# Optimization experiments

Hardware: AMD Instinct MI355X
Metric: run time of the kernel (lower is better)

## Reference

```python
import jax, jax.numpy as jnp
import numpy as np

B, S = 128, 512
VOCAB, E, H, T = 100000, 100, 128, 10  # tagset_size=10 -> CRF over T-1=9 tags
HD = H // 2  # per-direction LSTM hidden


def setup_inputs():
    key = jax.random.key(0)
    ks = jax.random.split(key, 14)
    s = 0.08
    inputs = jax.random.randint(ks[0], (B, S), 1, VOCAB)
    tags = jax.random.randint(ks[1], (B, S), 1, T)  # valid after tags-1 shift
    mask = jnp.ones((B, S), dtype=bool)
    emb = (jax.random.normal(ks[2], (VOCAB, E)) * s).at[0].set(0.0)  # padding_idx=0 row zeroed
    Wih_f = jax.random.normal(ks[3], (4 * HD, E)) * s
    Whh_f = jax.random.normal(ks[4], (4 * HD, HD)) * s
    b_f = jax.random.normal(ks[5], (4 * HD,)) * s
    Wih_b = jax.random.normal(ks[6], (4 * HD, E)) * s
    Whh_b = jax.random.normal(ks[7], (4 * HD, HD)) * s
    b_b = jax.random.normal(ks[8], (4 * HD,)) * s
    W_out = jax.random.normal(ks[9], (T, H)) * s
    b_out = jax.random.normal(ks[10], (T,)) * s
    start = jax.random.normal(ks[11], (T - 1,)) * s
    end = jax.random.normal(ks[12], (T - 1,)) * s
    trans = jax.random.normal(ks[13], (T - 1, T - 1)) * s
    return dict(inputs=inputs, tags=tags, mask=mask, emb=emb,
                Wih_f=Wih_f, Whh_f=Whh_f, b_f=b_f,
                Wih_b=Wih_b, Whh_b=Whh_b, b_b=b_b,
                W_out=W_out, b_out=b_out, start=start, end=end, trans=trans)


def _lstm_dir(x, Wih, Whh, b, reverse):
    # x: [S, B, E] time-major; PyTorch gate order i,f,g,o; b = b_ih + b_hh
    h0 = jnp.zeros((x.shape[1], Whh.shape[1]), x.dtype)

    def step(carry, xt):
        h, c = carry
        gates = xt @ Wih.T + h @ Whh.T + b
        i, f, g, o = jnp.split(gates, 4, axis=-1)
        c = jax.nn.sigmoid(f) * c + jax.nn.sigmoid(i) * jnp.tanh(g)
        h = jax.nn.sigmoid(o) * jnp.tanh(c)
        return (h, c), h

    _, hs = jax.lax.scan(step, (h0, h0), x, reverse=reverse)
    return hs  # [S, B, HD]


def _crf_nll(em, tags, mask, start, end, trans):
    # Linear-chain CRF (torchcrf-style). em: [S,B,K], tags/mask: [S,B]
    pick = lambda e, t: jnp.take_along_axis(e, t[:, None], axis=-1)[:, 0]
    # numerator: score of the gold path
    score0 = start[tags[0]] + pick(em[0], tags[0])

    def num_step(sc, inp):
        em_t, t, tp, m = inp
        return sc + jnp.where(m, trans[tp, t] + pick(em_t, t), 0.0), None

    score, _ = jax.lax.scan(num_step, score0, (em[1:], tags[1:], tags[:-1], mask[1:]))
    last_idx = mask.sum(0).astype(jnp.int32) - 1
    last_tags = jnp.take_along_axis(tags, last_idx[None, :], axis=0)[0]
    score = score + end[last_tags]
    # denominator: forward algorithm (log partition)
    alpha0 = start[None, :] + em[0]  # [B,K]

    def fwd_step(alpha, inp):
        em_t, m = inp
        nxt = jax.nn.logsumexp(alpha[:, :, None] + trans[None, :, :] + em_t[:, None, :], axis=1)
        return jnp.where(m[:, None], nxt, alpha), None

    alpha, _ = jax.lax.scan(fwd_step, alpha0, (em[1:], mask[1:]))
    logZ = jax.nn.logsumexp(alpha + end[None, :], axis=1)
    return -(score - logZ).mean()  # loss = -log_likelihood.mean()


def _forward(inputs, tags, mask, emb, Wih_f, Whh_f, b_f, Wih_b, Whh_b, b_b, W_out, b_out, start, end, trans):
    x = emb[inputs].transpose(1, 0, 2)  # [S,B,E]
    h = jnp.concatenate([_lstm_dir(x, Wih_f, Whh_f, b_f, False),
                         _lstm_dir(x, Wih_b, Whh_b, b_b, True)], axis=-1)  # [S,B,H]
    # dropout is identity at eval; slice off tag 0 as in the module
    em = (h @ W_out.T + b_out)[:, :, 1:]  # [S,B,T-1]
    return _crf_nll(em, (tags - 1).T, mask.T, start, end, trans)


def reference(inputs, tags, mask, emb, Wih_f, Whh_f, b_f, Wih_b, Whh_b, b_b, W_out, b_out, start, end, trans):
    return _forward(inputs, tags, mask, emb, Wih_f, Whh_f, b_f, Wih_b, Whh_b, b_b, W_out, b_out, start, end, trans)
```

## Files before the change

kernel.cpp:

```cpp
#include <hip/hip_runtime.h>
#include <math.h>

#define SB 512
#define NB 128
#define HD 64

typedef _Float16 h2 __attribute__((ext_vector_type(2)));
union U4 { uint4 u; h2 h[4]; _Float16 f[8]; };
union U2 { uint2 u; _Float16 f[4]; };
union UH { unsigned u; _Float16 f[2]; };

__device__ __forceinline__ float frcp(float x) { return __builtin_amdgcn_rcpf(x); }
__device__ __forceinline__ float fsig(float x) { return frcp(1.0f + __expf(-x)); }
__device__ __forceinline__ float ftanh(float x) {
    float t = __expf(-2.0f * fabsf(x));
    float r = (1.0f - t) * frcp(1.0f + t);
    return copysignf(r, x);
}
__device__ __forceinline__ float fdot2(h2 a, h2 b, float c) {
    return __builtin_amdgcn_fdot2(a, b, c, false);
}

__global__ void prep_kernel(const float* __restrict__ Wih_f, const float* __restrict__ Wih_bb,
                            const float* __restrict__ Whh_f, const float* __restrict__ Whh_bb,
                            const float* __restrict__ b_f, const float* __restrict__ b_bb,
                            const float* __restrict__ trans,
                            unsigned* __restrict__ W2h, unsigned* __restrict__ whh_h,
                            float* __restrict__ bias2, float* __restrict__ Eexp)
{
    int idx = blockIdx.x * 256 + threadIdx.x;
    if (idx < 26624) {
        int col = idx / 52, d = idx - col * 52;
        int dir = col >> 8, r = col & 255, j = r >> 2, g = r & 3;
        const float* src = (dir ? Wih_bb : Wih_f) + (g * 64 + j) * 100;
        UH u; u.u = 0;
        if (d < 50) { u.f[0] = (_Float16)src[2 * d]; u.f[1] = (_Float16)src[2 * d + 1]; }
        W2h[idx] = u.u;
    } else if (idx < 43008) {
        int i2 = idx - 26624;
        int q = i2 & 3, j = (i2 >> 2) & 63, k4 = (i2 >> 8) & 7, g = (i2 >> 11) & 3, dir = i2 >> 13;
        int p = k4 * 4 + q;
        const float* src = (dir ? Whh_bb : Whh_f) + (g * 64 + j) * 64 + 2 * p;
        UH u; u.f[0] = (_Float16)src[0]; u.f[1] = (_Float16)src[1];
        whh_h[(((dir * 4 + g) * 8 + k4) * 64 + j) * 4 + q] = u.u;
    } else if (idx < 43520) {
        int col = idx - 43008;
        int dir = col >> 8, r = col & 255, j = r >> 2, g = r & 3;
        bias2[col] = (dir ? b_bb : b_f)[g * 64 + j];
    } else if (idx < 43601) {
        int i = idx - 43520;
        Eexp[i] = __expf(trans[i]);
    }
}

__global__ __launch_bounds__(256, 1) void gemm_kernel(
    const int* __restrict__ inputs, const float* __restrict__ emb,
    const unsigned* __restrict__ W2h, const float* __restrict__ bias2,
    _Float16* __restrict__ xgh)
{
    __shared__ __align__(16) unsigned sE[128 * 52];
    __shared__ __align__(16) unsigned sW[128 * 52];
    __shared__ int stok[128];
    const int bx = blockIdx.x;
    const int tt = bx >> 2;
    const int cb = (bx & 3) * 128;
    const int tid = threadIdx.x;

    if (tid < 128) stok[tid] = inputs[tid * SB + tt];
    for (int idx = tid; idx < 1664; idx += 256)
        ((uint4*)sW)[idx] = ((const uint4*)W2h)[cb * 13 + idx];
    __syncthreads();
    for (int idx = tid; idx < 6656; idx += 256) {
        int row = idx / 52, d = idx - row * 52;
        int token = stok[row];
        UH u; u.u = 0;
        if (d < 50) {
            const float* ep = emb + (size_t)token * 100 + 2 * d;
            u.f[0] = (_Float16)ep[0]; u.f[1] = (_Float16)ep[1];
        }
        sE[idx] = u.u;
    }
    __syncthreads();

    const int tx = tid & 15, ty = tid >> 4;
    float acc[8][8];
    #pragma unroll
    for (int r = 0; r < 8; ++r)
        #pragma unroll
        for (int i = 0; i < 8; ++i) acc[r][i] = 0.f;

    for (int kk = 0; kk < 13; ++kk) {
        U4 e[8], wv[8];
        #pragma unroll
        for (int r = 0; r < 8; ++r) e[r].u = ((const uint4*)sE)[(ty + 16 * r) * 13 + kk];
        #pragma unroll
        for (int i = 0; i < 8; ++i) wv[i].u = ((const uint4*)sW)[(tx + 16 * i) * 13 + kk];
        #pragma unroll
        for (int r = 0; r < 8; ++r)
            #pragma unroll
            for (int i = 0; i < 8; ++i) {
                float a = acc[r][i];
                #pragma unroll
                for (int q = 0; q < 4; ++q) a = fdot2(e[r].h[q], wv[i].h[q], a);
                acc[r][i] = a;
            }
    }

    #pragma unroll
    for (int i = 0; i < 8; ++i) {
        int col = cb + tx + 16 * i;
        float bc = bias2[col];
        #pragma unroll
        for (int r = 0; r < 8; ++r) {
            int row = tt * NB + ty + 16 * r;
            xgh[(size_t)row * 512 + col] = (_Float16)(acc[r][i] + bc);
        }
    }
}

__global__ __launch_bounds__(64, 1) void lstm_kernel(
    const _Float16* __restrict__ xgh, const unsigned* __restrict__ whh_h,
    float* __restrict__ h_all)
{
    const int blk = blockIdx.x;
    const int b = blk & (NB - 1);
    const int dir = blk >> 7;
    const int j = threadIdx.x;

    U4 w[4][8];
    const uint4* W4 = (const uint4*)whh_h;
    #pragma unroll
    for (int g = 0; g < 4; ++g)
        #pragma unroll
        for (int k4 = 0; k4 < 8; ++k4)
            w[g][k4].u = W4[((dir * 4 + g) * 8 + k4) * 64 + j];

    __shared__ __align__(16) _Float16 hbuf[64];
    hbuf[j] = (_Float16)0.f;
    float c = 0.f;

    const int t0 = dir ? (SB - 1) : 0;
    const ptrdiff_t xstride = (dir ? -1 : 1) * (ptrdiff_t)(NB * 512);
    const ptrdiff_t hstride = (dir ? -1 : 1) * (ptrdiff_t)(NB * 128);
    const _Float16* xp = xgh + ((size_t)(t0 * NB + b)) * 512 + dir * 256 + j * 4;
    float* hp = h_all + ((size_t)(t0 * NB + b)) * 128 + dir * HD + j;

    U2 p0, p1;
    p0.u = *(const uint2*)xp;
    p1.u = *(const uint2*)(xp + xstride);
    const _Float16* xq = xp + 2 * xstride;
    __syncthreads();

    for (int s = 0; s < SB; ++s) {
        float a0 = (float)p0.f[0], a1 = (float)p0.f[1];
        float a2 = (float)p0.f[2], a3 = (float)p0.f[3];
        p0 = p1;
        p1.u = *(const uint2*)xq;
        xq += xstride;

        U4 hv[8];
        #pragma unroll
        for (int k4 = 0; k4 < 8; ++k4) hv[k4].u = ((const uint4*)hbuf)[k4];
        #pragma unroll
        for (int k4 = 0; k4 < 8; ++k4)
            #pragma unroll
            for (int q = 0; q < 4; ++q) {
                a0 = fdot2(hv[k4].h[q], w[0][k4].h[q], a0);
                a1 = fdot2(hv[k4].h[q], w[1][k4].h[q], a1);
                a2 = fdot2(hv[k4].h[q], w[2][k4].h[q], a2);
                a3 = fdot2(hv[k4].h[q], w[3][k4].h[q], a3);
            }

        float ig = fsig(a0), fg = fsig(a1), gg = ftanh(a2), og = fsig(a3);
        c = fg * c + ig * gg;
        float h = og * ftanh(c);
        *hp = h;
        hp += hstride;
        hbuf[j] = (_Float16)h;
        __syncthreads();
    }
}

__global__ __launch_bounds__(128) void proj_kernel(
    const float* __restrict__ h_all, const float* __restrict__ W_out,
    const float* __restrict__ b_out, float* __restrict__ em3)
{
    __shared__ __align__(16) float sWo[9 * 128];
    __shared__ float sb[9];
    const int t = blockIdx.x, b = threadIdx.x;
    for (int idx = b; idx < 1152; idx += 128) sWo[idx] = W_out[128 + idx];
    if (b < 9) sb[b] = b_out[1 + b];
    __syncthreads();

    const float4* h4 = (const float4*)(h_all + ((size_t)t * NB + b) * 128);
    float acc[9];
    #pragma unroll
    for (int k = 0; k < 9; ++k) acc[k] = 0.f;
    for (int q = 0; q < 32; ++q) {
        float4 hv = h4[q];
        #pragma unroll
        for (int k = 0; k < 9; ++k) {
            float4 wv = ((const float4*)sWo)[k * 32 + q];
            acc[k] += hv.x * wv.x + hv.y * wv.y + hv.z * wv.z + hv.w * wv.w;
        }
    }
    float* dst = em3 + (size_t)b * (SB * 12) + t * 12;
    #pragma unroll
    for (int k = 0; k < 9; ++k) dst[k] = acc[k] + sb[k];
}

__global__ __launch_bounds__(64, 1) void crf_gold(
    const float* __restrict__ em3, const int* __restrict__ tags,
    const float* __restrict__ startv, const float* __restrict__ endv,
    const float* __restrict__ trans, float* __restrict__ gold)
{
    const int b = blockIdx.x, l = threadIdx.x;
    const int* tb = tags + (size_t)b * SB;
    const float* eb = em3 + (size_t)b * (SB * 12);
    float sc = 0.f;
    for (int t = l; t < SB; t += 64) {
        int tg = tb[t] - 1;
        if (t > 0) {
            int tp = tb[t - 1] - 1;
            sc += trans[tp * 9 + tg] + eb[t * 12 + tg];
        }
    }
    if (l == 0) {
        int tg0 = tb[0] - 1, tgl = tb[SB - 1] - 1;
        sc += startv[tg0] + eb[tg0] + endv[tgl];
    }
    #pragma unroll
    for (int off = 32; off > 0; off >>= 1) sc += __shfl_down(sc, off);
    if (l == 0) gold[b] = sc;
}

__global__ __launch_bounds__(256, 1) void crf_scan(
    const float* __restrict__ em3, const float* __restrict__ Eexp,
    float* __restrict__ Pws)
{
    const int lane = blockIdx.x * 256 + threadIdx.x;
    const int c = lane & 31, b = lane >> 5;

    float E[81];
    #pragma unroll
    for (int i = 0; i < 81; ++i) E[i] = Eexp[i];

    float P[81];
    #pragma unroll
    for (int i = 0; i < 81; ++i) P[i] = 0.f;
    #pragma unroll
    for (int i = 0; i < 9; ++i) P[i * 9 + i] = 1.f;
    float M = 0.f;

    const int t0 = 1 + 16 * c;
    const int nst = (t0 + 16 <= SB) ? 16 : (SB - t0);
    const float* ep = em3 + (size_t)b * (SB * 12) + t0 * 12;

    for (int s = 0; s < nst; ++s, ep += 12) {
        float4 e0 = *(const float4*)ep;
        float4 e1 = *(const float4*)(ep + 4);
        float e8 = ep[8];
        float ex[9] = { __expf(e0.x), __expf(e0.y), __expf(e0.z), __expf(e0.w),
                        __expf(e1.x), __expf(e1.y), __expf(e1.z), __expf(e1.w),
                        __expf(e8) };
        #pragma unroll
        for (int i = 0; i < 9; ++i) {
            float tmp[9];
            #pragma unroll
            for (int jj = 0; jj < 9; ++jj) tmp[jj] = P[i * 9] * E[jj];
            #pragma unroll
            for (int k = 1; k < 9; ++k)
                #pragma unroll
                for (int jj = 0; jj < 9; ++jj) tmp[jj] += P[i * 9 + k] * E[k * 9 + jj];
            #pragma unroll
            for (int jj = 0; jj < 9; ++jj) P[i * 9 + jj] = tmp[jj] * ex[jj];
        }
        if ((s & 3) == 3) {
            float mx = P[0];
            #pragma unroll
            for (int i = 1; i < 81; ++i) mx = fmaxf(mx, P[i]);
            M += __logf(mx);
            float r = frcp(mx);
            #pragma unroll
            for (int i = 0; i < 81; ++i) P[i] *= r;
        }
    }

    float* dst = Pws + (size_t)lane * 84;
    #pragma unroll
    for (int i = 0; i < 81; ++i) dst[i] = P[i];
    dst[81] = M;
}

__global__ __launch_bounds__(128, 1) void crf_combine(
    const float* __restrict__ em3, const float* __restrict__ Pws,
    const float* __restrict__ gold, const float* __restrict__ startv,
    const float* __restrict__ endv, float* __restrict__ out)
{
    const int b = threadIdx.x;
    float A[9], M = 0.f;
    {
        const float* eb = em3 + (size_t)b * (SB * 12);
        float4 e0 = *(const float4*)eb;
        float4 e1 = *(const float4*)(eb + 4);
        float e[9] = { e0.x, e0.y, e0.z, e0.w, e1.x, e1.y, e1.z, e1.w, eb[8] };
        #pragma unroll
        for (int k = 0; k < 9; ++k) A[k] = __expf(startv[k] + e[k]);
    }

    for (int c = 0; c < 32; ++c) {
        const float4* src = (const float4*)(Pws + ((size_t)b * 32 + c) * 84);
        float buf[84];
        #pragma unroll
        for (int q = 0; q < 21; ++q) {
            float4 v = src[q];
            buf[4 * q] = v.x; buf[4 * q + 1] = v.y; buf[4 * q + 2] = v.z; buf[4 * q + 3] = v.w;
        }
        float tmp[9];
        #pragma unroll
        for (int jj = 0; jj < 9; ++jj) tmp[jj] = A[0] * buf[jj];
        #pragma unroll
        for (int i = 1; i < 9; ++i)
            #pragma unroll
            for (int jj = 0; jj < 9; ++jj) tmp[jj] += A[i] * buf[i * 9 + jj];
        float mx = tmp[0];
        #pragma unroll
        for (int jj = 1; jj < 9; ++jj) mx = fmaxf(mx, tmp[jj]);
        M += __logf(mx) + buf[81];
        float r = frcp(mx);
        #pragma unroll
        for (int jj = 0; jj < 9; ++jj) A[jj] = tmp[jj] * r;
    }

    float Z = 0.f;
    #pragma unroll
    for (int k = 0; k < 9; ++k) Z += A[k] * __expf(endv[k]);
    float part = M + __logf(Z) - gold[b];

    #pragma unroll
    for (int off = 32; off > 0; off >>= 1) part += __shfl_down(part, off);
    __shared__ float sm[2];
    if ((b & 63) == 0) sm[b >> 6] = part;
    __syncthreads();
    if (b == 0) out[0] = (sm[0] + sm[1]) * (1.0f / NB);
}

extern "C" void kernel_launch(void* const* d_in, const int* in_sizes, int n_in,
                              void* d_out, int out_size, void* d_ws, size_t ws_size,
                              hipStream_t stream)
{
    const int*   inputs = (const int*)d_in[0];
    const int*   tags   = (const int*)d_in[1];
    const float* emb    = (const float*)d_in[3];
    const float* Wih_f  = (const float*)d_in[4];
    const float* Whh_f  = (const float*)d_in[5];
    const float* b_f    = (const float*)d_in[6];
    const float* Wih_b  = (const float*)d_in[7];
    const float* Whh_b  = (const float*)d_in[8];
    const float* b_b    = (const float*)d_in[9];
    const float* W_out  = (const float*)d_in[10];
    const float* b_out  = (const float*)d_in[11];
    const float* startv = (const float*)d_in[12];
    const float* endv   = (const float*)d_in[13];
    const float* transv = (const float*)d_in[14];

    char* w = (char*)d_ws;
    float* h_all   = (float*)w;     w += (size_t)SB * NB * 128 * 4;
    _Float16* xgh  = (_Float16*)w;  w += (size_t)SB * NB * 512 * 2;
    float* em3     = (float*)w;     w += (size_t)NB * SB * 12 * 4;
    float* Pws     = (float*)w;     w += (size_t)NB * 32 * 84 * 4;
    float* gold    = (float*)w;     w += NB * 4;
    unsigned* W2h  = (unsigned*)w;  w += 26624 * 4;
    unsigned* whh  = (unsigned*)w;  w += 16384 * 4;
    float* bias2   = (float*)w;     w += 512 * 4;
    float* Eexp    = (float*)w;     w += 81 * 4;

    prep_kernel<<<171, 256, 0, stream>>>(Wih_f, Wih_b, Whh_f, Whh_b, b_f, b_b, transv,
                                         W2h, whh, bias2, Eexp);
    gemm_kernel<<<2048, 256, 0, stream>>>(inputs, emb, W2h, bias2, xgh);
    lstm_kernel<<<256, 64, 0, stream>>>(xgh, whh, h_all);
    proj_kernel<<<SB, 128, 0, stream>>>(h_all, W_out, b_out, em3);
    crf_gold<<<NB, 64, 0, stream>>>(em3, tags, startv, endv, transv, gold);
    crf_scan<<<16, 256, 0, stream>>>(em3, Eexp, Pws);
    crf_combine<<<1, 128, 0, stream>>>(em3, Pws, gold, startv, endv, (float*)d_out);
}
```

Before: 531.0 us.

## Run LSTM recurrence with MFMA over 16-batch groups and fragment-ordered gate inputs

The recurrent LSTM kernel now processes 16 sequences per workgroup with four waves, computing h@Whh with 16x16x32 f16 MFMA instructions instead of per-thread fdot2 loops over a single sequence. The input-gate GEMM writes its output directly in the MFMA accumulator fragment layout so each lane loads its gate inputs with two vector loads per step. Hidden state is double-buffered in padded shared memory, and Whh is converted to f16 inside the LSTM kernel rather than in prep. The grid shrinks from 256 to 16 workgroups, so the serial recurrence runs on far fewer CUs and depends on MFMA latency per step.

```diff
diff --git a/kernel.cpp b/kernel.cpp
--- a/kernel.cpp
+++ b/kernel.cpp
@@ -6,9 +6,11 @@
 #define HD 64
 
 typedef _Float16 h2 __attribute__((ext_vector_type(2)));
+typedef _Float16 half8 __attribute__((ext_vector_type(8)));
+typedef float floatx4 __attribute__((ext_vector_type(4)));
 union U4 { uint4 u; h2 h[4]; _Float16 f[8]; };
-union U2 { uint2 u; _Float16 f[4]; };
 union UH { unsigned u; _Float16 f[2]; };
+union PU { uint4 u[2]; _Float16 f[16]; };
 
 __device__ __forceinline__ float frcp(float x) { return __builtin_amdgcn_rcpf(x); }
 __device__ __forceinline__ float fsig(float x) { return frcp(1.0f + __expf(-x)); }
@@ -22,11 +24,10 @@
 }
 
 __global__ void prep_kernel(const float* __restrict__ Wih_f, const float* __restrict__ Wih_bb,
-                            const float* __restrict__ Whh_f, const float* __restrict__ Whh_bb,
                             const float* __restrict__ b_f, const float* __restrict__ b_bb,
                             const float* __restrict__ trans,
-                            unsigned* __restrict__ W2h, unsigned* __restrict__ whh_h,
-                            float* __restrict__ bias2, float* __restrict__ Eexp)
+                            unsigned* __restrict__ W2h, float* __restrict__ bias2,
+                            float* __restrict__ Eexp)
 {
     int idx = blockIdx.x * 256 + threadIdx.x;
     if (idx < 26624) {
@@ -36,19 +37,12 @@
         UH u; u.u = 0;
         if (d < 50) { u.f[0] = (_Float16)src[2 * d]; u.f[1] = (_Float16)src[2 * d + 1]; }
         W2h[idx] = u.u;
-    } else if (idx < 43008) {
-        int i2 = idx - 26624;
-        int q = i2 & 3, j = (i2 >> 2) & 63, k4 = (i2 >> 8) & 7, g = (i2 >> 11) & 3, dir = i2 >> 13;
-        int p = k4 * 4 + q;
-        const float* src = (dir ? Whh_bb : Whh_f) + (g * 64 + j) * 64 + 2 * p;
-        UH u; u.f[0] = (_Float16)src[0]; u.f[1] = (_Float16)src[1];
-        whh_h[(((dir * 4 + g) * 8 + k4) * 64 + j) * 4 + q] = u.u;
-    } else if (idx < 43520) {
-        int col = idx - 43008;
+    } else if (idx < 27136) {
+        int col = idx - 26624;
         int dir = col >> 8, r = col & 255, j = r >> 2, g = r & 3;
         bias2[col] = (dir ? b_bb : b_f)[g * 64 + j];
-    } else if (idx < 43601) {
-        int i = idx - 43520;
+    } else if (idx < 27217) {
+        int i = idx - 27136;
         Eexp[i] = __expf(trans[i]);
     }
 }
@@ -56,7 +50,7 @@
 __global__ __launch_bounds__(256, 1) void gemm_kernel(
     const int* __restrict__ inputs, const float* __restrict__ emb,
     const unsigned* __restrict__ W2h, const float* __restrict__ bias2,
-    _Float16* __restrict__ xgh)
+    _Float16* __restrict__ xgF)
 {
     __shared__ __align__(16) unsigned sE[128 * 52];
     __shared__ __align__(16) unsigned sW[128 * 52];
@@ -108,75 +102,101 @@
 
     #pragma unroll
     for (int i = 0; i < 8; ++i) {
-        int col = cb + tx + 16 * i;
-        float bc = bias2[col];
+        int gcol = cb + tx + 16 * i;
+        float bc = bias2[gcol];
+        int dirq = gcol >> 8, rr = gcol & 255, u = rr >> 2, g = rr & 3;
+        int ww = u >> 4, cc = u & 15;
         #pragma unroll
         for (int r = 0; r < 8; ++r) {
-            int row = tt * NB + ty + 16 * r;
-            xgh[(size_t)row * 512 + col] = (_Float16)(acc[r][i] + bc);
-        }
-    }
-}
-
-__global__ __launch_bounds__(64, 1) void lstm_kernel(
-    const _Float16* __restrict__ xgh, const unsigned* __restrict__ whh_h,
+            int batch = ty + 16 * r;
+            int grp = batch >> 4, bi = batch & 15;
+            int ln = ((bi >> 2) << 4) | cc;
+            size_t addr = (((size_t)tt * 2 + dirq) * 8 + grp) * 4096
+                          + ww * 1024 + ln * 16 + g * 4 + (bi & 3);
+            xgF[addr] = (_Float16)(acc[r][i] + bc);
+        }
+    }
+}
+
+__global__ __launch_bounds__(256, 1) void lstm_kernel(
+    const _Float16* __restrict__ xgF,
+    const float* __restrict__ Whh_f, const float* __restrict__ Whh_bb,
     float* __restrict__ h_all)
 {
     const int blk = blockIdx.x;
-    const int b = blk & (NB - 1);
-    const int dir = blk >> 7;
-    const int j = threadIdx.x;
-
-    U4 w[4][8];
-    const uint4* W4 = (const uint4*)whh_h;
+    const int dir = blk & 1, grp = blk >> 1;
+    const int tid = threadIdx.x;
+    const int w = tid >> 6, lane = tid & 63;
+    const int c = lane & 15, quad = lane >> 4;
+    const float* Whh = dir ? Whh_bb : Whh_f;
+
+    half8 Bf[4][2];
     #pragma unroll
     for (int g = 0; g < 4; ++g)
         #pragma unroll
-        for (int k4 = 0; k4 < 8; ++k4)
-            w[g][k4].u = W4[((dir * 4 + g) * 8 + k4) * 64 + j];
-
-    __shared__ __align__(16) _Float16 hbuf[64];
-    hbuf[j] = (_Float16)0.f;
-    float c = 0.f;
-
+        for (int kh = 0; kh < 2; ++kh) {
+            const float* src = Whh + (g * 64 + 16 * w + c) * 64 + kh * 32 + quad * 8;
+            half8 v;
+            #pragma unroll
+            for (int j = 0; j < 8; ++j) v[j] = (_Float16)src[j];
+            Bf[g][kh] = v;
+        }
+
+    __shared__ __align__(16) _Float16 hb[2][16][72];
+    for (int i = tid; i < 2 * 16 * 72; i += 256) ((_Float16*)hb)[i] = (_Float16)0.f;
+
+    float cst[4] = {0.f, 0.f, 0.f, 0.f};
+    const int u = 16 * w + c;
+
+    const ptrdiff_t tstep = (dir ? -1 : 1) * (ptrdiff_t)(65536 / 8);
     const int t0 = dir ? (SB - 1) : 0;
-    const ptrdiff_t xstride = (dir ? -1 : 1) * (ptrdiff_t)(NB * 512);
-    const ptrdiff_t hstride = (dir ? -1 : 1) * (ptrdiff_t)(NB * 128);
-    const _Float16* xp = xgh + ((size_t)(t0 * NB + b)) * 512 + dir * 256 + j * 4;
-    float* hp = h_all + ((size_t)(t0 * NB + b)) * 128 + dir * HD + j;
-
-    U2 p0, p1;
-    p0.u = *(const uint2*)xp;
-    p1.u = *(const uint2*)(xp + xstride);
-    const _Float16* xq = xp + 2 * xstride;
+    const uint4* xp = (const uint4*)xgF
+        + (((size_t)t0 * 2 + dir) * 8 + grp) * 512 + w * 128 + lane * 2;
+    PU p0, p1;
+    p0.u[0] = xp[0]; p0.u[1] = xp[1];
+    xp += tstep;
+    p1.u[0] = xp[0]; p1.u[1] = xp[1];
+    xp += tstep;
     __syncthreads();
 
     for (int s = 0; s < SB; ++s) {
-        float a0 = (float)p0.f[0], a1 = (float)p0.f[1];
-        float a2 = (float)p0.f[2], a3 = (float)p0.f[3];
+        const int t = dir ? (SB - 1 - s) : s;
+
+        floatx4 accv[4];
+        #pragma unroll
+        for (int g = 0; g < 4; ++g) {
+            floatx4 ci;
+            #pragma unroll
+            for (int r = 0; r < 4; ++r) ci[r] = (float)p0.f[g * 4 + r];
+            accv[g] = ci;
+        }
         p0 = p1;
-        p1.u = *(const uint2*)xq;
-        xq += xstride;
-
-        U4 hv[8];
-        #pragma unroll
-        for (int k4 = 0; k4 < 8; ++k4) hv[k4].u = ((const uint4*)hbuf)[k4];
-        #pragma unroll
-        for (int k4 = 0; k4 < 8; ++k4)
-            #pragma unroll
-            for (int q = 0; q < 4; ++q) {
-                a0 = fdot2(hv[k4].h[q], w[0][k4].h[q], a0);
-                a1 = fdot2(hv[k4].h[q], w[1][k4].h[q], a1);
-                a2 = fdot2(hv[k4].h[q], w[2][k4].h[q], a2);
-                a3 = fdot2(hv[k4].h[q], w[3][k4].h[q], a3);
-            }
-
-        float ig = fsig(a0), fg = fsig(a1), gg = ftanh(a2), og = fsig(a3);
-        c = fg * c + ig * gg;
-        float h = og * ftanh(c);
-        *hp = h;
-        hp += hstride;
-        hbuf[j] = (_Float16)h;
+        p1.u[0] = xp[0]; p1.u[1] = xp[1];
+        xp += tstep;
+
+        const int rbuf = s & 1;
+        half8 a0 = *(const half8*)&hb[rbuf][c][quad * 8];
+        half8 a1 = *(const half8*)&hb[rbuf][c][32 + quad * 8];
+
+        #pragma unroll
+        for (int g = 0; g < 4; ++g) {
+            accv[g] = __builtin_amdgcn_mfma_f32_16x16x32_f16(a0, Bf[g][0], accv[g], 0, 0, 0);
+            accv[g] = __builtin_amdgcn_mfma_f32_16x16x32_f16(a1, Bf[g][1], accv[g], 0, 0, 0);
+        }
+
+        const int wbuf = (s + 1) & 1;
+        #pragma unroll
+        for (int r = 0; r < 4; ++r) {
+            float ig = fsig(accv[0][r]);
+            float fg = fsig(accv[1][r]);
+            float gg = ftanh(accv[2][r]);
+            float og = fsig(accv[3][r]);
+            float cc2 = fg * cst[r] + ig * gg;
+            cst[r] = cc2;
+            float h = og * ftanh(cc2);
+            hb[wbuf][quad * 4 + r][u] = (_Float16)h;
+            h_all[(((size_t)t * NB) + grp * 16 + quad * 4 + r) * 128 + dir * HD + u] = h;
+        }
         __syncthreads();
     }
 }
@@ -365,20 +385,18 @@
     const float* transv = (const float*)d_in[14];
 
     char* w = (char*)d_ws;
+    float* em3     = (float*)w;     w += (size_t)NB * SB * 12 * 4;
+    _Float16* xgF  = (_Float16*)w;  w += (size_t)SB * 65536 * 2;
     float* h_all   = (float*)w;     w += (size_t)SB * NB * 128 * 4;
-    _Float16* xgh  = (_Float16*)w;  w += (size_t)SB * NB * 512 * 2;
-    float* em3     = (float*)w;     w += (size_t)NB * SB * 12 * 4;
     float* Pws     = (float*)w;     w += (size_t)NB * 32 * 84 * 4;
     float* gold    = (float*)w;     w += NB * 4;
     unsigned* W2h  = (unsigned*)w;  w += 26624 * 4;
-    unsigned* whh  = (unsigned*)w;  w += 16384 * 4;
     float* bias2   = (float*)w;     w += 512 * 4;
     float* Eexp    = (float*)w;     w += 81 * 4;
 
-    prep_kernel<<<171, 256, 0, stream>>>(Wih_f, Wih_b, Whh_f, Whh_b, b_f, b_b, transv,
-                                         W2h, whh, bias2, Eexp);
-    gemm_kernel<<<2048, 256, 0, stream>>>(inputs, emb, W2h, bias2, xgh);
-    lstm_kernel<<<256, 64, 0, stream>>>(xgh, whh, h_all);
+    prep_kernel<<<107, 256, 0, stream>>>(Wih_f, Wih_b, b_f, b_b, transv, W2h, bias2, Eexp);
+    gemm_kernel<<<2048, 256, 0, stream>>>(inputs, emb, W2h, bias2, xgF);
+    lstm_kernel<<<16, 256, 0, stream>>>(xgF, Whh_f, Whh_b, h_all);
     proj_kernel<<<SB, 128, 0, stream>>>(h_all, W_out, b_out, em3);
     crf_gold<<<NB, 64, 0, stream>>>(em3, tags, startv, endv, transv, gold);
     crf_scan<<<16, 256, 0, stream>>>(em3, Eexp, Pws);
```

Measured after the change: 622.0 us. 17.1% more time.

## Store LSTM hidden states as fp16 per-batch layout and retile projection

Applied to the files above, without the earlier changes.

The LSTM kernel now writes hidden states as fp16 in a batch-major, per-direction layout instead of fp32 time-major. It also uses four independent partial accumulators per gate to shorten the fdot2 dependency chain, and pins the recurrent weights in registers. The projection kernel is rewritten to run one block per batch row, staging 128-timestep tiles in shared memory and using fp16 dot products. This cuts the bytes written and read for hidden states and lowers serial latency per recurrence step, at the cost of fp16 rounding of the projection inputs.

```diff
diff --git a/kernel.cpp b/kernel.cpp
--- a/kernel.cpp
+++ b/kernel.cpp
@@ -25,7 +25,7 @@
                             const float* __restrict__ Whh_f, const float* __restrict__ Whh_bb,
                             const float* __restrict__ b_f, const float* __restrict__ b_bb,
                             const float* __restrict__ trans,
-                            unsigned* __restrict__ W2h, unsigned* __restrict__ whh_h,
+                            unsigned* __restrict__ W2h, unsigned* __restrict__ whh16,
                             float* __restrict__ bias2, float* __restrict__ Eexp)
 {
     int idx = blockIdx.x * 256 + threadIdx.x;
@@ -37,12 +37,11 @@
         if (d < 50) { u.f[0] = (_Float16)src[2 * d]; u.f[1] = (_Float16)src[2 * d + 1]; }
         W2h[idx] = u.u;
     } else if (idx < 43008) {
-        int i2 = idx - 26624;
-        int q = i2 & 3, j = (i2 >> 2) & 63, k4 = (i2 >> 8) & 7, g = (i2 >> 11) & 3, dir = i2 >> 13;
-        int p = k4 * 4 + q;
-        const float* src = (dir ? Whh_bb : Whh_f) + (g * 64 + j) * 64 + 2 * p;
-        UH u; u.f[0] = (_Float16)src[0]; u.f[1] = (_Float16)src[1];
-        whh_h[(((dir * 4 + g) * 8 + k4) * 64 + j) * 4 + q] = u.u;
+        int d = idx - 26624;
+        int kp = d & 31, u = (d >> 5) & 63, g = (d >> 11) & 3, dir = d >> 13;
+        const float* src = (dir ? Whh_bb : Whh_f) + (g * 64 + u) * 64 + 2 * kp;
+        UH uu; uu.f[0] = (_Float16)src[0]; uu.f[1] = (_Float16)src[1];
+        whh16[d] = uu.u;
     } else if (idx < 43520) {
         int col = idx - 43008;
         int dir = col >> 8, r = col & 255, j = r >> 2, g = r & 3;
@@ -119,21 +118,24 @@
 }
 
 __global__ __launch_bounds__(64, 1) void lstm_kernel(
-    const _Float16* __restrict__ xgh, const unsigned* __restrict__ whh_h,
-    float* __restrict__ h_all)
+    const _Float16* __restrict__ xgh, const unsigned* __restrict__ whh16,
+    _Float16* __restrict__ h16)
 {
     const int blk = blockIdx.x;
     const int b = blk & (NB - 1);
     const int dir = blk >> 7;
     const int j = threadIdx.x;
 
-    U4 w[4][8];
-    const uint4* W4 = (const uint4*)whh_h;
+    U4 w[32];
+    const uint4* W4 = (const uint4*)(whh16 + dir * 8192);
     #pragma unroll
     for (int g = 0; g < 4; ++g)
         #pragma unroll
         for (int k4 = 0; k4 < 8; ++k4)
-            w[g][k4].u = W4[((dir * 4 + g) * 8 + k4) * 64 + j];
+            w[g * 8 + k4].u = W4[(g * 64 + j) * 8 + k4];
+    #pragma unroll
+    for (int i = 0; i < 32; ++i)
+        asm volatile("" : "+v"(w[i].u.x), "+v"(w[i].u.y), "+v"(w[i].u.z), "+v"(w[i].u.w));
 
     __shared__ __align__(16) _Float16 hbuf[64];
     hbuf[j] = (_Float16)0.f;
@@ -141,9 +143,9 @@
 
     const int t0 = dir ? (SB - 1) : 0;
     const ptrdiff_t xstride = (dir ? -1 : 1) * (ptrdiff_t)(NB * 512);
-    const ptrdiff_t hstride = (dir ? -1 : 1) * (ptrdiff_t)(NB * 128);
     const _Float16* xp = xgh + ((size_t)(t0 * NB + b)) * 512 + dir * 256 + j * 4;
-    float* hp = h_all + ((size_t)(t0 * NB + b)) * 128 + dir * HD + j;
+    _Float16* hp = h16 + ((size_t)(b * 2 + dir) * SB + t0) * 64 + j;
+    const ptrdiff_t hstride = (dir ? -1 : 1) * (ptrdiff_t)64;
 
     U2 p0, p1;
     p0.u = *(const uint2*)xp;
@@ -160,53 +162,88 @@
 
         U4 hv[8];
         #pragma unroll
-        for (int k4 = 0; k4 < 8; ++k4) hv[k4].u = ((const uint4*)hbuf)[k4];
-        #pragma unroll
-        for (int k4 = 0; k4 < 8; ++k4)
+        for (int k4 = 0; k4 < 8; ++k4) hv[k4].u = *(const uint4*)&hbuf[k4 * 8];
+
+        float g0[4] = {a0, 0.f, 0.f, 0.f};
+        float g1[4] = {a1, 0.f, 0.f, 0.f};
+        float g2[4] = {a2, 0.f, 0.f, 0.f};
+        float g3[4] = {a3, 0.f, 0.f, 0.f};
+        #pragma unroll
+        for (int k4 = 0; k4 < 8; ++k4) {
+            const int p = k4 & 3;
             #pragma unroll
             for (int q = 0; q < 4; ++q) {
-                a0 = fdot2(hv[k4].h[q], w[0][k4].h[q], a0);
-                a1 = fdot2(hv[k4].h[q], w[1][k4].h[q], a1);
-                a2 = fdot2(hv[k4].h[q], w[2][k4].h[q], a2);
-                a3 = fdot2(hv[k4].h[q], w[3][k4].h[q], a3);
+                g0[p] = fdot2(hv[k4].h[q], w[0 * 8 + k4].h[q], g0[p]);
+                g1[p] = fdot2(hv[k4].h[q], w[1 * 8 + k4].h[q], g1[p]);
+                g2[p] = fdot2(hv[k4].h[q], w[2 * 8 + k4].h[q], g2[p]);
+                g3[p] = fdot2(hv[k4].h[q], w[3 * 8 + k4].h[q], g3[p]);
             }
+        }
+        a0 = (g0[0] + g0[1]) + (g0[2] + g0[3]);
+        a1 = (g1[0] + g1[1]) + (g1[2] + g1[3]);
+        a2 = (g2[0] + g2[1]) + (g2[2] + g2[3]);
+        a3 = (g3[0] + g3[1]) + (g3[2] + g3[3]);
 
         float ig = fsig(a0), fg = fsig(a1), gg = ftanh(a2), og = fsig(a3);
         c = fg * c + ig * gg;
         float h = og * ftanh(c);
-        *hp = h;
+        *hp = (_Float16)h;
         hp += hstride;
         hbuf[j] = (_Float16)h;
         __syncthreads();
     }
 }
 
-__global__ __launch_bounds__(128) void proj_kernel(
-    const float* __restrict__ h_all, const float* __restrict__ W_out,
+__global__ __launch_bounds__(256, 1) void proj_kernel(
+    const _Float16* __restrict__ h16, const float* __restrict__ W_out,
     const float* __restrict__ b_out, float* __restrict__ em3)
 {
-    __shared__ __align__(16) float sWo[9 * 128];
+    __shared__ __align__(16) unsigned tile[128 * 64];
+    __shared__ __align__(16) unsigned sWo[9 * 64];
     __shared__ float sb[9];
-    const int t = blockIdx.x, b = threadIdx.x;
-    for (int idx = b; idx < 1152; idx += 128) sWo[idx] = W_out[128 + idx];
-    if (b < 9) sb[b] = b_out[1 + b];
-    __syncthreads();
-
-    const float4* h4 = (const float4*)(h_all + ((size_t)t * NB + b) * 128);
-    float acc[9];
-    #pragma unroll
-    for (int k = 0; k < 9; ++k) acc[k] = 0.f;
-    for (int q = 0; q < 32; ++q) {
-        float4 hv = h4[q];
-        #pragma unroll
-        for (int k = 0; k < 9; ++k) {
-            float4 wv = ((const float4*)sWo)[k * 32 + q];
-            acc[k] += hv.x * wv.x + hv.y * wv.y + hv.z * wv.z + hv.w * wv.w;
-        }
-    }
-    float* dst = em3 + (size_t)b * (SB * 12) + t * 12;
-    #pragma unroll
-    for (int k = 0; k < 9; ++k) dst[k] = acc[k] + sb[k];
+    const int b = blockIdx.x, tid = threadIdx.x;
+
+    for (int i2 = tid; i2 < 576; i2 += 256) {
+        int k = i2 >> 6, jp = i2 & 63;
+        const float* src = W_out + (k + 1) * 128 + 2 * jp;
+        UH u; u.f[0] = (_Float16)src[0]; u.f[1] = (_Float16)src[1];
+        sWo[i2] = u.u;
+    }
+    if (tid < 9) sb[tid] = b_out[1 + tid];
+
+    float* dst0 = em3 + (size_t)b * (SB * 12);
+
+    for (int tt = 0; tt < 4; ++tt) {
+        const int t0 = tt * 128;
+        __syncthreads();
+        #pragma unroll
+        for (int dir = 0; dir < 2; ++dir) {
+            const unsigned* src = (const unsigned*)(h16 + ((size_t)(b * 2 + dir) * SB + t0) * 64);
+            for (int i = tid; i < 4096; i += 256) {
+                int t = i >> 5, jp = i & 31;
+                tile[t * 64 + dir * 32 + jp] = src[i];
+            }
+        }
+        __syncthreads();
+
+        for (int o = tid; o < 1152; o += 256) {
+            int tl = o / 9, k = o - 9 * tl;
+            const U4* hr = (const U4*)&tile[tl * 64];
+            const U4* wr = (const U4*)&sWo[k * 64];
+            float pa = 0.f, pb = 0.f;
+            #pragma unroll
+            for (int q = 0; q < 16; q += 2) {
+                U4 hv = hr[q], wv = wr[q];
+                U4 hv2 = hr[q + 1], wv2 = wr[q + 1];
+                #pragma unroll
+                for (int z = 0; z < 4; ++z) {
+                    pa = fdot2(hv.h[z], wv.h[z], pa);
+                    pb = fdot2(hv2.h[z], wv2.h[z], pb);
+                }
+            }
+            dst0[(t0 + tl) * 12 + k] = pa + pb + sb[k];
+        }
+    }
 }
 
 __global__ __launch_bounds__(64, 1) void crf_gold(
@@ -365,21 +402,21 @@
     const float* transv = (const float*)d_in[14];
 
     char* w = (char*)d_ws;
-    float* h_all   = (float*)w;     w += (size_t)SB * NB * 128 * 4;
+    float* em3     = (float*)w;     w += (size_t)NB * SB * 12 * 4;
     _Float16* xgh  = (_Float16*)w;  w += (size_t)SB * NB * 512 * 2;
-    float* em3     = (float*)w;     w += (size_t)NB * SB * 12 * 4;
+    _Float16* h16  = (_Float16*)w;  w += (size_t)NB * 2 * SB * 64 * 2;
     float* Pws     = (float*)w;     w += (size_t)NB * 32 * 84 * 4;
     float* gold    = (float*)w;     w += NB * 4;
     unsigned* W2h  = (unsigned*)w;  w += 26624 * 4;
-    unsigned* whh  = (unsigned*)w;  w += 16384 * 4;
+    unsigned* whh16= (unsigned*)w;  w += 16384 * 4;
     float* bias2   = (float*)w;     w += 512 * 4;
     float* Eexp    = (float*)w;     w += 81 * 4;
 
     prep_kernel<<<171, 256, 0, stream>>>(Wih_f, Wih_b, Whh_f, Whh_b, b_f, b_b, transv,
-                                         W2h, whh, bias2, Eexp);
+                                         W2h, whh16, bias2, Eexp);
     gemm_kernel<<<2048, 256, 0, stream>>>(inputs, emb, W2h, bias2, xgh);
-    lstm_kernel<<<256, 64, 0, stream>>>(xgh, whh, h_all);
-    proj_kernel<<<SB, 128, 0, stream>>>(h_all, W_out, b_out, em3);
+    lstm_kernel<<<256, 64, 0, stream>>>(xgh, whh16, h16);
+    proj_kernel<<<NB, 256, 0, stream>>>(h16, W_out, b_out, em3);
     crf_gold<<<NB, 64, 0, stream>>>(em3, tags, startv, endv, transv, gold);
     crf_scan<<<16, 256, 0, stream>>>(em3, Eexp, Pws);
     crf_combine<<<1, 128, 0, stream>>>(em3, Pws, gold, startv, endv, (float*)d_out);
```

Result: slower. 666.1 us (+25.4%).
